# Optimization experiments

Measured on AMD Instinct MI355X. Metric: run time of the kernel, lower is better.

Reference implementation:

```python
import jax, jax.numpy as jnp
import numpy as np

N_HEAD = 16
D_MODEL = 1024

def setup_inputs() -> dict:
    key = jax.random.key(0)
    ks = jax.random.split(key, 9)
    B, S, D = 8, 1024, D_MODEL
    scale = 1.0 / np.sqrt(D)
    inp = {
        'q': jax.random.normal(ks[0], (B, S, D), jnp.float32),
        'k': jax.random.normal(ks[1], (B, S, D), jnp.float32),
        'v': jax.random.normal(ks[2], (B, S, D), jnp.float32),
        'w_q': jax.random.normal(ks[3], (D, D), jnp.float32) * scale,
        'b_q': jnp.zeros((D,), jnp.float32),
        'w_k': jax.random.normal(ks[4], (D, D), jnp.float32) * scale,
        'b_k': jnp.zeros((D,), jnp.float32),
        'w_v': jax.random.normal(ks[5], (D, D), jnp.float32) * scale,
        'b_v': jnp.zeros((D,), jnp.float32),
    }
    return inp

def reference(q, k, v, w_q, b_q, w_k, b_k, w_v, b_v):
    B, S, D = q.shape
    H = N_HEAD
    dk = D // H
    # QKV projections, split into heads: [B, S, D] -> [B, H, S, dk]
    def proj(x, w, b):
        return (x @ w + b).reshape(B, S, H, dk).transpose(0, 2, 1, 3)
    qh = proj(q, w_q, b_q)
    kh = proj(k, w_k, b_k)
    vh = proj(v, w_v, b_v)
    # scaled dot-product attention (attention matrix materialized as in source)
    scores = jnp.einsum('bhqd,bhkd->bhqk', qh, kh) / jnp.sqrt(jnp.asarray(dk, q.dtype))
    attn = jax.nn.softmax(scores, axis=-1)
    # dropout disabled (eval mode)
    out = jnp.einsum('bhqk,bhkd->bhqd', attn, vh)  # [B, H, S, dk]
    return out.transpose(0, 2, 1, 3).reshape(B, S, D)
```

## Files before the change

### kernel.cpp

```cpp
#include <hip/hip_runtime.h>
#include <hip/hip_bf16.h>

#define BB 8
#define SS 1024
#define DD 1024
#define HH 16
#define DK 64
#define MM (BB*SS)

typedef __attribute__((ext_vector_type(8))) short bf16x8;
typedef __attribute__((ext_vector_type(4))) short bf16x4;
typedef __attribute__((ext_vector_type(4))) float f32x4;
typedef __attribute__((ext_vector_type(4))) int i32x4;

#define QSCALE 0.18033688011112042f
#define SBIAS -12.0f

static __device__ __forceinline__ short f2bf(float f) {
    union { float f; unsigned u; } x; x.f = f;
    unsigned r = x.u + 0x7fffu + ((x.u >> 16) & 1u);
    return (short)(r >> 16);
}

#define GLOAD16(g, s) __builtin_amdgcn_global_load_lds( \
    (const __attribute__((address_space(1))) void*)(g), \
    (__attribute__((address_space(3))) void*)(s), 16, 0, 0)

__global__ void wtrans_kernel(const float* __restrict__ w0, const float* __restrict__ w1,
                              const float* __restrict__ w2, short* __restrict__ wt) {
    __shared__ short t[32][33];
    int p = blockIdx.z;
    const float* wsrc = p == 0 ? w0 : (p == 1 ? w1 : w2);
    short* dst = wt + (size_t)p * DD * DD;
    int k0 = blockIdx.y * 32, n0 = blockIdx.x * 32;
    int tx = threadIdx.x & 31, ty = threadIdx.x >> 5;
    #pragma unroll
    for (int i = 0; i < 4; ++i) {
        int k = ty + 8 * i;
        t[k][tx] = f2bf(wsrc[(size_t)(k0 + k) * DD + n0 + tx]);
    }
    __syncthreads();
    #pragma unroll
    for (int i = 0; i < 4; ++i) {
        int n = ty + 8 * i;
        dst[(size_t)(n0 + n) * DD + k0 + tx] = t[tx][n];
    }
}

__global__ void xcast_kernel(const float* __restrict__ xq, const float* __restrict__ xk,
                             const float* __restrict__ xv, short* __restrict__ xbf) {
    int z = blockIdx.y;
    const float* src = z == 0 ? xq : (z == 1 ? xk : xv);
    size_t i = ((size_t)blockIdx.x * 256 + threadIdx.x) * 8;
    f32x4 a = *(const f32x4*)(src + i);
    f32x4 b = *(const f32x4*)(src + i + 4);
    bf16x8 pk;
    pk[0] = f2bf(a[0]); pk[1] = f2bf(a[1]); pk[2] = f2bf(a[2]); pk[3] = f2bf(a[3]);
    pk[4] = f2bf(b[0]); pk[5] = f2bf(b[1]); pk[6] = f2bf(b[2]); pk[7] = f2bf(b[3]);
    *(bf16x8*)(xbf + (size_t)z * MM * DD + i) = pk;
}

#define BM 128
#define BN 128
#define BK 64

template<int ABF16>
__launch_bounds__(256, 3)
__global__ void qkvproj_kernel(const float* __restrict__ xq, const float* __restrict__ xk,
                               const float* __restrict__ xv,
                               const short* __restrict__ xbf,
                               const short* __restrict__ wt,
                               const float* __restrict__ bq, const float* __restrict__ bk,
                               const float* __restrict__ bv,
                               short* __restrict__ qh, short* __restrict__ kh,
                               short* __restrict__ vh) {
    __shared__ short As[BM * 64];
    __shared__ short Bs[BN * 64];
    int lin = blockIdx.x + 8 * (blockIdx.y + 64 * blockIdx.z);
    int sz = (lin & 7) * 192 + (lin >> 3);
    int p = sz >> 9;
    int n0 = (sz & 7) * BN;
    int m0 = ((sz >> 3) & 63) * BM;
    const float* X = p == 0 ? xq : (p == 1 ? xk : xv);
    const short* Wt = wt + (size_t)p * DD * DD;
    const float* bias = p == 0 ? bq : (p == 1 ? bk : bv);
    short* out = p == 0 ? qh : (p == 1 ? kh : vh);
    int t = threadIdx.x;
    int l = t & 63, w = t >> 6;
    int wm = (w >> 1) * 64, wn = (w & 1) * 64;
    int lg = l >> 4, lr = l & 15;
    int rx = lr & 7;

    f32x4 acc[4][4];
    #pragma unroll
    for (int mi = 0; mi < 4; ++mi)
        #pragma unroll
        for (int ni = 0; ni < 4; ++ni) acc[mi][ni] = 0.f;

    for (int k0 = 0; k0 < DD; k0 += BK) {
        __syncthreads();
        if constexpr (ABF16) {
            const short* Xb = xbf + (size_t)p * MM * DD;
            #pragma unroll
            for (int j = 0; j < 4; ++j) {
                int chunk = j * 256 + t;
                int row = chunk >> 3, seg = chunk & 7;
                const short* src = Xb + (size_t)(m0 + row) * DD + k0 + ((seg ^ (row & 7)) * 8);
                GLOAD16(src, &As[(j * 256 + w * 64) * 8]);
            }
        } else {
            #pragma unroll
            for (int i = 0; i < 4; ++i) {
                int c = t + 256 * i;
                int row = c >> 3, seg = c & 7;
                const float* src = X + (size_t)(m0 + row) * DD + k0 + seg * 8;
                f32x4 f0 = *(const f32x4*)(src);
                f32x4 f1 = *(const f32x4*)(src + 4);
                bf16x8 pk;
                pk[0] = f2bf(f0[0]); pk[1] = f2bf(f0[1]); pk[2] = f2bf(f0[2]); pk[3] = f2bf(f0[3]);
                pk[4] = f2bf(f1[0]); pk[5] = f2bf(f1[1]); pk[6] = f2bf(f1[2]); pk[7] = f2bf(f1[3]);
                *(bf16x8*)(&As[row * 64 + ((seg ^ (row & 7)) * 8)]) = pk;
            }
        }
        #pragma unroll
        for (int j = 0; j < 4; ++j) {
            int chunk = j * 256 + t;
            int row = chunk >> 3, seg = chunk & 7;
            const short* src = Wt + (size_t)(n0 + row) * DD + k0 + ((seg ^ (row & 7)) * 8);
            GLOAD16(src, &Bs[(j * 256 + w * 64) * 8]);
        }
        __syncthreads();
        #pragma unroll
        for (int kk = 0; kk < 2; ++kk) {
            bf16x8 a[4], b[4];
            #pragma unroll
            for (int mi = 0; mi < 4; ++mi)
                a[mi] = *(const bf16x8*)(&As[(wm + mi * 16 + lr) * 64 + (((kk * 4 + lg) ^ rx) * 8)]);
            #pragma unroll
            for (int ni = 0; ni < 4; ++ni)
                b[ni] = *(const bf16x8*)(&Bs[(wn + ni * 16 + lr) * 64 + (((kk * 4 + lg) ^ rx) * 8)]);
            #pragma unroll
            for (int mi = 0; mi < 4; ++mi)
                #pragma unroll
                for (int ni = 0; ni < 4; ++ni)
                    acc[mi][ni] = __builtin_amdgcn_mfma_f32_16x16x32_bf16(a[mi], b[ni], acc[mi][ni], 0, 0, 0);
        }
    }
    float osc = (p == 0) ? QSCALE : 1.0f;
    #pragma unroll
    for (int ni = 0; ni < 4; ++ni) {
        int n = n0 + wn + ni * 16 + lr;
        float bvv = bias[n];
        int h = n >> 6, dd = n & 63;
        #pragma unroll
        for (int mi = 0; mi < 4; ++mi) {
            int mbase = m0 + wm + mi * 16 + lg * 4;
            #pragma unroll
            for (int r = 0; r < 4; ++r) {
                int m = mbase + r;
                int b_ = m >> 10, s_ = m & 1023;
                out[(((size_t)(b_ * HH + h) * SS + s_) * DK) + dd] = f2bf((acc[mi][ni][r] + bvv) * osc);
            }
        }
    }
}

__global__ void vtrans_kernel(const short* __restrict__ vh, short* __restrict__ vt) {
    __shared__ short tile[64 * 72];
    int bh = blockIdx.y;
    int s0 = blockIdx.x * 64;
    int t = threadIdx.x;
    #pragma unroll
    for (int i = 0; i < 2; ++i) {
        int c = t + 256 * i;
        int row = c >> 3, dc = (c & 7) * 8;
        *(bf16x8*)&tile[row * 72 + dc] =
            *(const bf16x8*)(vh + ((size_t)bh * SS + s0 + row) * DK + dc);
    }
    __syncthreads();
    #pragma unroll
    for (int i = 0; i < 2; ++i) {
        int c = t + 256 * i;
        int dr = c >> 3, scc = (c & 7) * 8;
        bf16x8 vv;
        #pragma unroll
        for (int j = 0; j < 8; ++j) vv[j] = tile[(scc + j) * 72 + dr];
        *(bf16x8*)(vt + ((size_t)bh * DK + dr) * SS + s0 + scc) = vv;
    }
}


#define SOFTMAX_PV(KT, VT, AQ0, AQ1, OO, OS) {                              \
    f32x4 sc[4];                                                            \
    __builtin_amdgcn_s_setprio(1);                                          \
    _Pragma("unroll")                                                       \
    for (int ct = 0; ct < 4; ++ct) {                                        \
        int row = ct * 16 + lr;                                             \
        bf16x8 k0 = *(const bf16x8*)&KT[row * 64 + ((lg ^ sw) * 8)];        \
        bf16x8 k1 = *(const bf16x8*)&KT[row * 64 + (((lg + 4) ^ sw) * 8)];  \
        f32x4 z = { SBIAS, SBIAS, SBIAS, SBIAS };                           \
        z = __builtin_amdgcn_mfma_f32_16x16x32_bf16(k0, AQ0, z, 0, 0, 0);   \
        z = __builtin_amdgcn_mfma_f32_16x16x32_bf16(k1, AQ1, z, 0, 0, 0);   \
        sc[ct] = z;                                                         \
    }                                                                       \
    __builtin_amdgcn_s_setprio(0);                                          \
    float p_[4][4];                                                         \
    _Pragma("unroll")                                                       \
    for (int ct = 0; ct < 4; ++ct) {                                        \
        p_[ct][0] = exp2f(sc[ct][0]);                                       \
        p_[ct][1] = exp2f(sc[ct][1]);                                       \
        p_[ct][2] = exp2f(sc[ct][2]);                                       \
        p_[ct][3] = exp2f(sc[ct][3]);                                       \
    }                                                                       \
    unsigned X00, X01, X10, X11, X20, X21, X30, X31;                        \
    asm("v_cvt_pk_bf16_f32 %0, %1, %2" : "=v"(X00) : "v"(p_[0][0]), "v"(p_[0][1])); \
    asm("v_cvt_pk_bf16_f32 %0, %1, %2" : "=v"(X01) : "v"(p_[0][2]), "v"(p_[0][3])); \
    asm("v_cvt_pk_bf16_f32 %0, %1, %2" : "=v"(X10) : "v"(p_[1][0]), "v"(p_[1][1])); \
    asm("v_cvt_pk_bf16_f32 %0, %1, %2" : "=v"(X11) : "v"(p_[1][2]), "v"(p_[1][3])); \
    asm("v_cvt_pk_bf16_f32 %0, %1, %2" : "=v"(X20) : "v"(p_[2][0]), "v"(p_[2][1])); \
    asm("v_cvt_pk_bf16_f32 %0, %1, %2" : "=v"(X21) : "v"(p_[2][2]), "v"(p_[2][3])); \
    asm("v_cvt_pk_bf16_f32 %0, %1, %2" : "=v"(X30) : "v"(p_[3][0]), "v"(p_[3][1])); \
    asm("v_cvt_pk_bf16_f32 %0, %1, %2" : "=v"(X31) : "v"(p_[3][2]), "v"(p_[3][3])); \
    auto r0 = __builtin_amdgcn_permlane32_swap((int)X00, (int)X10, false, false); \
    auto r1 = __builtin_amdgcn_permlane32_swap((int)X01, (int)X11, false, false); \
    auto r2 = __builtin_amdgcn_permlane32_swap((int)X20, (int)X30, false, false); \
    auto r3 = __builtin_amdgcn_permlane32_swap((int)X21, (int)X31, false, false); \
    i32x4 pa0i = { (int)r0[0], (int)r1[0], (int)r0[1], (int)r1[1] };        \
    i32x4 pa1i = { (int)r2[0], (int)r3[0], (int)r2[1], (int)r3[1] };        \
    bf16x8 pa0 = __builtin_bit_cast(bf16x8, pa0i);                          \
    bf16x8 pa1 = __builtin_bit_cast(bf16x8, pa1i);                          \
    __builtin_amdgcn_s_setprio(1);                                          \
    _Pragma("unroll")                                                       \
    for (int dt = 0; dt < 4; ++dt) {                                        \
        int row = dt * 16 + lr;                                             \
        bf16x8 v0 = *(const bf16x8*)&VT[row * 64 + ((lg ^ sw) * 8)];        \
        bf16x8 v1 = *(const bf16x8*)&VT[row * 64 + (((lg + 4) ^ sw) * 8)];  \
        OO[dt] = __builtin_amdgcn_mfma_f32_16x16x32_bf16(pa0, v0, OO[dt], 0, 0, 0); \
        OO[dt] = __builtin_amdgcn_mfma_f32_16x16x32_bf16(pa1, v1, OO[dt], 0, 0, 0); \
    }                                                                       \
    OS = __builtin_amdgcn_mfma_f32_16x16x32_bf16(pa0, vones, OS, 0, 0, 0);  \
    OS = __builtin_amdgcn_mfma_f32_16x16x32_bf16(pa1, vones, OS, 0, 0, 0);  \
    __builtin_amdgcn_s_setprio(0);                                          \
}

__launch_bounds__(256, 4)
__global__ void attn_kernel(const short* __restrict__ qh, const short* __restrict__ kh,
                            const short* __restrict__ vt, float* __restrict__ out) {
    __shared__ short KBuf[2][64 * 64];
    __shared__ short VBuf[2][64 * 64];
    int lin = blockIdx.y * 8 + blockIdx.x;
    int swz = (lin & 7) * 128 + (lin >> 3);
    int bh = swz >> 3;
    int q0 = (swz & 7) * 128;
    int t = threadIdx.x, l = t & 63, w = t >> 6;
    int lg = l >> 4, lr = l & 15;
    int sw = lr & 7;
    const short* Q  = qh + (size_t)bh * SS * DK;
    const short* Kg = kh + (size_t)bh * SS * DK;
    const short* Vg = vt + (size_t)bh * DK * SS;

    bf16x8 vones;
    #pragma unroll
    for (int i = 0; i < 8; ++i) vones[i] = (short)0x3F80;

    int qrow = q0 + w * 32 + lr;
    bf16x8 aq00 = *(const bf16x8*)(Q + (size_t)qrow * DK + lg * 8);
    bf16x8 aq01 = *(const bf16x8*)(Q + (size_t)qrow * DK + 32 + lg * 8);
    bf16x8 aq10 = *(const bf16x8*)(Q + (size_t)(qrow + 16) * DK + lg * 8);
    bf16x8 aq11 = *(const bf16x8*)(Q + (size_t)(qrow + 16) * DK + 32 + lg * 8);

    f32x4 o0[4], o1[4], os0, os1;
    #pragma unroll
    for (int dt = 0; dt < 4; ++dt) { o0[dt] = 0.f; o1[dt] = 0.f; }
    os0 = 0.f; os1 = 0.f;

#define STAGE_KV(kv, b) { \
    _Pragma("unroll") \
    for (int j = 0; j < 2; ++j) { \
        int c = (j * 4 + w) * 64 + l; \
        int row = c >> 3, s = c & 7; \
        int rowg = (row & ~12) | ((row & 4) << 1) | ((row & 8) >> 1); \
        GLOAD16(Kg + (size_t)((kv) + rowg) * DK + ((s ^ (row & 7)) * 8), \
                &KBuf[b][(j * 4 + w) * 512]); \
        GLOAD16(Vg + (size_t)row * SS + (kv) + ((s ^ (row & 7)) * 8), \
                &VBuf[b][(j * 4 + w) * 512]); \
    } }

    STAGE_KV(0, 0);
    __syncthreads();

    for (int tt = 0; tt < 16; ++tt) {
        int cur = tt & 1;
        if (tt < 15) STAGE_KV((tt + 1) * 64, cur ^ 1);
        const short* KT = &KBuf[cur][0];
        const short* VT = &VBuf[cur][0];
        SOFTMAX_PV(KT, VT, aq00, aq01, o0, os0);
        SOFTMAX_PV(KT, VT, aq10, aq11, o1, os1);
        __syncthreads();
    }
#undef STAGE_KV

    int b_ = bh >> 4, h_ = bh & 15;
    #pragma unroll
    for (int r = 0; r < 4; ++r) {
        float inv0 = 1.0f / os0[r];
        int srow0 = q0 + w * 32 + lg * 4 + r;
        float* op0 = out + ((size_t)(b_ * SS + srow0)) * DD + h_ * DK;
        #pragma unroll
        for (int dt = 0; dt < 4; ++dt)
            op0[dt * 16 + lr] = o0[dt][r] * inv0;
        float inv1 = 1.0f / os1[r];
        int srow1 = srow0 + 16;
        float* op1 = out + ((size_t)(b_ * SS + srow1)) * DD + h_ * DK;
        #pragma unroll
        for (int dt = 0; dt < 4; ++dt)
            op1[dt * 16 + lr] = o1[dt][r] * inv1;
    }
}

extern "C" void kernel_launch(void* const* d_in, const int* in_sizes, int n_in,
                              void* d_out, int out_size, void* d_ws, size_t ws_size,
                              hipStream_t stream) {
    const float* q  = (const float*)d_in[0];
    const float* k  = (const float*)d_in[1];
    const float* v  = (const float*)d_in[2];
    const float* wq = (const float*)d_in[3];
    const float* bq = (const float*)d_in[4];
    const float* wk = (const float*)d_in[5];
    const float* bk = (const float*)d_in[6];
    const float* wv = (const float*)d_in[7];
    const float* bv = (const float*)d_in[8];
    float* out = (float*)d_out;

    char* ws = (char*)d_ws;
    const size_t SZ = (size_t)BB * HH * SS * DK * sizeof(short);
    short* Qh = (short*)(ws);
    short* Kh = (short*)(ws + SZ);
    short* Vh = (short*)(ws + 2 * SZ);
    short* Vt = (short*)(ws + 3 * SZ);
    short* Wt = (short*)(ws + 4 * SZ);
    const size_t XOFF = 4 * SZ + 3 * (size_t)DD * DD * sizeof(short);
    short* Xbf = (short*)(ws + XOFF);
    const size_t need = XOFF + 3 * (size_t)MM * DD * sizeof(short);

    wtrans_kernel<<<dim3(32, 32, 3), 256, 0, stream>>>(wq, wk, wv, Wt);
    if (ws_size >= need) {
        xcast_kernel<<<dim3(MM * DD / (256 * 8), 3), 256, 0, stream>>>(q, k, v, Xbf);
        qkvproj_kernel<1><<<dim3(8, 64, 3), 256, 0, stream>>>(q, k, v, Xbf, Wt, bq, bk, bv, Qh, Kh, Vh);
    } else {
        qkvproj_kernel<0><<<dim3(8, 64, 3), 256, 0, stream>>>(q, k, v, nullptr, Wt, bq, bk, bv, Qh, Kh, Vh);
    }
    vtrans_kernel<<<dim3(16, 128), 256, 0, stream>>>(Vh, Vt);
    attn_kernel<<<dim3(8, 128), 256, 0, stream>>>(Qh, Kh, Vt, out);
}
```

Baseline: 144.6 us.

## Split attention block into eight waves each owning sixteen query rows

Moves the attention kernel from 256 to 512 threads per block, giving each wave 16 query rows instead of 32. The per-wave accumulators and Q fragments are halved, and K/V staging now uses one 16-byte load per thread rather than two. The aim is more waves in flight and lower register pressure to hide latency. The trade-off is that each K/V tile loaded into LDS is amortised over fewer MFMA ops per wave, and the block-wide barrier now synchronises more waves.

```diff
diff --git a/kernel.cpp b/kernel.cpp
--- a/kernel.cpp
+++ b/kernel.cpp
@@ -243,7 +243,7 @@
     __builtin_amdgcn_s_setprio(0);                                          \
 }
 
-__launch_bounds__(256, 4)
+__launch_bounds__(512, 6)
 __global__ void attn_kernel(const short* __restrict__ qh, const short* __restrict__ kh,
                             const short* __restrict__ vt, float* __restrict__ out) {
     __shared__ short KBuf[2][64 * 64];
@@ -263,28 +263,24 @@
     #pragma unroll
     for (int i = 0; i < 8; ++i) vones[i] = (short)0x3F80;
 
-    int qrow = q0 + w * 32 + lr;
-    bf16x8 aq00 = *(const bf16x8*)(Q + (size_t)qrow * DK + lg * 8);
-    bf16x8 aq01 = *(const bf16x8*)(Q + (size_t)qrow * DK + 32 + lg * 8);
-    bf16x8 aq10 = *(const bf16x8*)(Q + (size_t)(qrow + 16) * DK + lg * 8);
-    bf16x8 aq11 = *(const bf16x8*)(Q + (size_t)(qrow + 16) * DK + 32 + lg * 8);
-
-    f32x4 o0[4], o1[4], os0, os1;
-    #pragma unroll
-    for (int dt = 0; dt < 4; ++dt) { o0[dt] = 0.f; o1[dt] = 0.f; }
-    os0 = 0.f; os1 = 0.f;
+    int qrow = q0 + w * 16 + lr;
+    bf16x8 aq0 = *(const bf16x8*)(Q + (size_t)qrow * DK + lg * 8);
+    bf16x8 aq1 = *(const bf16x8*)(Q + (size_t)qrow * DK + 32 + lg * 8);
+
+    f32x4 o[4], os;
+    #pragma unroll
+    for (int dt = 0; dt < 4; ++dt) o[dt] = 0.f;
+    os = 0.f;
 
 #define STAGE_KV(kv, b) { \
-    _Pragma("unroll") \
-    for (int j = 0; j < 2; ++j) { \
-        int c = (j * 4 + w) * 64 + l; \
-        int row = c >> 3, s = c & 7; \
-        int rowg = (row & ~12) | ((row & 4) << 1) | ((row & 8) >> 1); \
-        GLOAD16(Kg + (size_t)((kv) + rowg) * DK + ((s ^ (row & 7)) * 8), \
-                &KBuf[b][(j * 4 + w) * 512]); \
-        GLOAD16(Vg + (size_t)row * SS + (kv) + ((s ^ (row & 7)) * 8), \
-                &VBuf[b][(j * 4 + w) * 512]); \
-    } }
+    int c = t; \
+    int row = c >> 3, s = c & 7; \
+    int rowg = (row & ~12) | ((row & 4) << 1) | ((row & 8) >> 1); \
+    GLOAD16(Kg + (size_t)((kv) + rowg) * DK + ((s ^ (row & 7)) * 8), \
+            &KBuf[b][w * 512]); \
+    GLOAD16(Vg + (size_t)row * SS + (kv) + ((s ^ (row & 7)) * 8), \
+            &VBuf[b][w * 512]); \
+    }
 
     STAGE_KV(0, 0);
     __syncthreads();
@@ -294,8 +290,7 @@
         if (tt < 15) STAGE_KV((tt + 1) * 64, cur ^ 1);
         const short* KT = &KBuf[cur][0];
         const short* VT = &VBuf[cur][0];
-        SOFTMAX_PV(KT, VT, aq00, aq01, o0, os0);
-        SOFTMAX_PV(KT, VT, aq10, aq11, o1, os1);
+        SOFTMAX_PV(KT, VT, aq0, aq1, o, os);
         __syncthreads();
     }
 #undef STAGE_KV
@@ -303,18 +298,12 @@
     int b_ = bh >> 4, h_ = bh & 15;
     #pragma unroll
     for (int r = 0; r < 4; ++r) {
-        float inv0 = 1.0f / os0[r];
-        int srow0 = q0 + w * 32 + lg * 4 + r;
-        float* op0 = out + ((size_t)(b_ * SS + srow0)) * DD + h_ * DK;
+        float inv = 1.0f / os[r];
+        int srow = q0 + w * 16 + lg * 4 + r;
+        float* op = out + ((size_t)(b_ * SS + srow)) * DD + h_ * DK;
         #pragma unroll
         for (int dt = 0; dt < 4; ++dt)
-            op0[dt * 16 + lr] = o0[dt][r] * inv0;
-        float inv1 = 1.0f / os1[r];
-        int srow1 = srow0 + 16;
-        float* op1 = out + ((size_t)(b_ * SS + srow1)) * DD + h_ * DK;
-        #pragma unroll
-        for (int dt = 0; dt < 4; ++dt)
-            op1[dt * 16 + lr] = o1[dt][r] * inv1;
+            op[dt * 16 + lr] = o[dt][r] * inv;
     }
 }
 
@@ -351,5 +340,5 @@
         qkvproj_kernel<0><<<dim3(8, 64, 3), 256, 0, stream>>>(q, k, v, nullptr, Wt, bq, bk, bv, Qh, Kh, Vh);
     }
     vtrans_kernel<<<dim3(16, 128), 256, 0, stream>>>(Vh, Vt);
-    attn_kernel<<<dim3(8, 128), 256, 0, stream>>>(Qh, Kh, Vt, out);
-}
+    attn_kernel<<<dim3(8, 128), 512, 0, stream>>>(Qh, Kh, Vt, out);
+}
```

Result: no change. 143.9 us (median of 2 runs) (-0.5%).
